# Optimization experiments

Hardware: AMD Instinct MI355X
Metric: run time of the kernel (lower is better)

## Reference

```python
import jax, jax.numpy as jnp
import numpy as np

NUM_HEADS = 6
ATTN_TH = 0.0
NEG_INF = -10000.0  # masked-score fill for threshold pruning


def setup_inputs() -> dict:
    key = jax.random.key(0)
    k1, k2, k3 = jax.random.split(key, 3)
    B, N, C = 8, 1024, 384
    x = jax.random.normal(k1, (B, N, C), dtype=jnp.float32)
    # Linear weights (torch layout: [out, in]), scaled like default init
    w_qkv = jax.random.normal(k2, (3 * C, C), dtype=jnp.float32) * (1.0 / np.sqrt(C))
    b_qkv = jnp.zeros((3 * C,), dtype=jnp.float32)
    w_proj = jax.random.normal(k3, (C, C), dtype=jnp.float32) * (1.0 / np.sqrt(C))
    b_proj = jnp.zeros((C,), dtype=jnp.float32)
    return {"x": x, "w_qkv": w_qkv, "b_qkv": b_qkv, "w_proj": w_proj, "b_proj": b_proj}


def reference(x, w_qkv, b_qkv, w_proj, b_proj):
    B, N, C = x.shape
    H = NUM_HEADS
    D = C // H
    scale = D ** -0.5
    # QAct nodes are identity (quant=False); QLinear is a plain linear.
    qkv = jnp.einsum('bnc,oc->bno', x, w_qkv) + b_qkv          # [B,N,3C]
    qkv = qkv.reshape(B, N, 3, H, D).transpose(2, 0, 3, 1, 4)   # [3,B,H,N,D]
    q, k, v = qkv[0], qkv[1], qkv[2]
    attn = jnp.einsum('bhnd,bhmd->bhnm', q, k) * scale          # [B,H,N,N]
    # Threshold pruning: scores below Attn_Th are masked out of the softmax.
    attn = jnp.where(attn < ATTN_TH, NEG_INF, attn)
    attn = jax.nn.softmax(attn, axis=-1)
    out = jnp.einsum('bhnm,bhmd->bhnd', attn, v)                # [B,H,N,D]
    out = out.transpose(0, 2, 1, 3).reshape(B, N, C)
    out = jnp.einsum('bnc,oc->bno', out, w_proj) + b_proj
    return out
```

## Files before the change

### kernel.cpp

```cpp
#include <hip/hip_runtime.h>
#include <hip/hip_bf16.h>


typedef __attribute__((__ext_vector_type__(8))) __bf16 bf16x8;
typedef __attribute__((__ext_vector_type__(8))) unsigned short ushort8;
typedef __attribute__((__ext_vector_type__(4))) unsigned short ushort4v;
typedef __attribute__((__ext_vector_type__(4))) short short4v;
typedef __attribute__((__ext_vector_type__(4))) float f32x4;

#define NX 3145728
#define NQ 442368
#define NP 147456

__device__ __forceinline__ f32x4 mfma32(bf16x8 a, bf16x8 b, f32x4 c) {
    return __builtin_amdgcn_mfma_f32_16x16x32_bf16(a, b, c, 0, 0, 0);
}
__device__ __forceinline__ f32x4 mfma16(short4v a, short4v b, f32x4 c) {
    return __builtin_amdgcn_mfma_f32_16x16x16bf16_1k(a, b, c, 0, 0, 0);
}

__device__ __forceinline__ unsigned short f2bf(float f) {
    union { float f; unsigned int i; } x; x.f = f;
    unsigned int u = x.i;
    return (unsigned short)((u + 0x7fffu + ((u >> 16) & 1u)) >> 16);
}

__device__ __forceinline__ void dma16(const unsigned short* g, unsigned short* l) {
    __builtin_amdgcn_global_load_lds(
        (const __attribute__((address_space(1))) unsigned int*)g,
        (__attribute__((address_space(3))) unsigned int*)l, 16, 0, 0);
}

__global__ __launch_bounds__(256) void cvt_bf16(
    const float* __restrict__ x, const float* __restrict__ wq, const float* __restrict__ wp,
    unsigned short* __restrict__ xb, unsigned short* __restrict__ wqb, unsigned short* __restrict__ wpb)
{
    int i = blockIdx.x * 256 + threadIdx.x;
    const float* src; unsigned short* dst; int off;
    if (i < NX / 4)              { src = x;  dst = xb;  off = i * 4; }
    else if (i < (NX + NQ) / 4)  { src = wq; dst = wqb; off = i * 4 - NX; }
    else                         { src = wp; dst = wpb; off = i * 4 - NX - NQ; }
    float4 v = *(const float4*)(src + off);
    ushort4v r;
    r[0] = f2bf(v.x); r[1] = f2bf(v.y); r[2] = f2bf(v.z); r[3] = f2bf(v.w);
    *(ushort4v*)(dst + off) = r;
}

template <int MODE, int TM>
__global__ __launch_bounds__(TM * 2) void gemm_bt(
    const unsigned short* __restrict__ A,
    const unsigned short* __restrict__ B,
    const float* __restrict__ bias,
    unsigned short* __restrict__ qg,
    unsigned short* __restrict__ kg,
    unsigned short* __restrict__ vg,
    float* __restrict__ out,
    int M, int N, int K)
{
    const int tid  = threadIdx.x;
    const int lane = tid & 63;
    const int wave = tid >> 6;
    const int l15  = lane & 15;
    const int quad = lane >> 4;
    const int m0 = blockIdx.x * TM;
    const int n0 = blockIdx.y * 128;
    const int wm = (wave >> 1) * 64;
    const int wn = (wave & 1) * 64;

    __shared__ __align__(16) unsigned short As[TM * 32];
    __shared__ __align__(16) unsigned short Bs[128 * 32];

    f32x4 acc[4][4];
    #pragma unroll
    for (int i = 0; i < 4; ++i)
        #pragma unroll
        for (int j = 0; j < 4; ++j)
            acc[i][j] = (f32x4){0.f, 0.f, 0.f, 0.f};

    for (int k0 = 0; k0 < K; k0 += 32) {
        #pragma unroll
        for (int t = 0; t < 2; ++t) {
            int i = tid + t * TM * 2;
            dma16(A + (size_t)(m0 + (i >> 2)) * K + k0 + (i & 3) * 8,
                  As + t * TM * 16 + wave * 512);
        }
        #pragma unroll
        for (int t = 0; t < 512 / (TM * 2); ++t) {
            int i = tid + t * TM * 2;
            dma16(B + (size_t)(n0 + (i >> 2)) * K + k0 + (i & 3) * 8,
                  Bs + t * TM * 16 + wave * 512);
        }
        __syncthreads();

        bf16x8 af[4], bff[4];
        #pragma unroll
        for (int mt = 0; mt < 4; ++mt)
            af[mt] = *(const bf16x8*)(As + (wm + mt * 16 + l15) * 32 + quad * 8);
        #pragma unroll
        for (int nt = 0; nt < 4; ++nt)
            bff[nt] = *(const bf16x8*)(Bs + (wn + nt * 16 + l15) * 32 + quad * 8);
        #pragma unroll
        for (int mt = 0; mt < 4; ++mt)
            #pragma unroll
            for (int nt = 0; nt < 4; ++nt)
                acc[mt][nt] = mfma32(af[mt], bff[nt], acc[mt][nt]);
        __syncthreads();
    }

    if constexpr (MODE == 0) {
        if (n0 < 384) {
            #pragma unroll
            for (int nt = 0; nt < 4; ++nt) {
                int n = n0 + wn + nt * 16 + l15;
                float bv = bias[n];
                #pragma unroll
                for (int mt = 0; mt < 4; ++mt) {
                    int mbase = m0 + wm + mt * 16 + quad * 4;
                    #pragma unroll
                    for (int r = 0; r < 4; ++r)
                        qg[(size_t)(mbase + r) * 384 + n] = f2bf((acc[mt][nt][r] + bv) * 0.125f);
                }
            }
        } else if (n0 < 768) {
            #pragma unroll
            for (int nt = 0; nt < 4; ++nt) {
                int n = n0 + wn + nt * 16 + l15;
                float bv = bias[n];
                int c2 = n - 384;
                int h = c2 >> 6, ck = c2 & 63;
                int half = ck >> 5, qd = (ck >> 3) & 3, j = ck & 7;
                #pragma unroll
                for (int mt = 0; mt < 4; ++mt) {
                    int mbase = m0 + wm + mt * 16 + quad * 4;
                    #pragma unroll
                    for (int r = 0; r < 4; ++r) {
                        int tok = mbase + r;
                        int b = tok >> 10, kv = tok & 1023;
                        int kt = kv >> 4, lk = kv & 15;
                        kg[(size_t)(b * 6 + h) * 65536 +
                           ((((size_t)kt * 2 + half) * 4 + qd) * 16 + lk) * 8 + j]
                            = f2bf(acc[mt][nt][r] + bv);
                    }
                }
            }
        } else {
            #pragma unroll
            for (int nt = 0; nt < 4; ++nt) {
                int n = n0 + wn + nt * 16 + l15;
                float bv = bias[n];
                int c2 = n - 768;
                int h = c2 >> 6, d = c2 & 63;
                int dt = d >> 4, lv = d & 15;
                #pragma unroll
                for (int mt = 0; mt < 4; ++mt) {
                    int mbase = m0 + wm + mt * 16 + quad * 4;
                    int b = mbase >> 10, kvb = mbase & 1023;
                    int cc = kvb >> 6, jt = (kvb >> 4) & 3, qd = (kvb >> 2) & 3;
                    ushort4v pk;
                    #pragma unroll
                    for (int r = 0; r < 4; ++r) pk[r] = f2bf(acc[mt][nt][r] + bv);
                    *(ushort4v*)(vg + (size_t)(b * 6 + h) * 65536 + (size_t)cc * 4096 +
                                 (((jt * 4 + dt) * 4 + qd) * 16 + lv) * 4) = pk;
                }
            }
        }
    } else {
        #pragma unroll
        for (int nt = 0; nt < 4; ++nt) {
            int n = n0 + wn + nt * 16 + l15;
            float bv = bias[n];
            #pragma unroll
            for (int mt = 0; mt < 4; ++mt) {
                int mbase = m0 + wm + mt * 16 + quad * 4;
                #pragma unroll
                for (int r = 0; r < 4; ++r)
                    out[(size_t)(mbase + r) * N + n] = acc[mt][nt][r] + bv;
            }
        }
    }
}

__global__ __launch_bounds__(256) void attn_fused(
    const unsigned short* __restrict__ qg,
    const unsigned short* __restrict__ kg,
    const unsigned short* __restrict__ vg,
    unsigned short* __restrict__ aout)
{
    const int tid  = threadIdx.x;
    const int wave = tid >> 6;
    const int lane = tid & 63;
    const int l15  = lane & 15;
    const int quad = lane >> 4;
    const int qt = blockIdx.x;
    const int h  = blockIdx.y;
    const int b  = blockIdx.z;

    const size_t rowbase = (size_t)b * 1024;
    const unsigned short* Kslab = kg + (size_t)(b * 6 + h) * 65536;
    const unsigned short* Vslab = vg + (size_t)(b * 6 + h) * 65536;
    const int q0 = qt * 64 + wave * 16;

    __shared__ __align__(16) unsigned short Kb[4096];
    __shared__ __align__(16) unsigned short Vb[4096];

    bf16x8 aq0, aq1;
    {
        const unsigned short* qrow = qg + (rowbase + q0 + l15) * 384 + h * 64 + quad * 8;
        aq0 = *(const bf16x8*)qrow;
        aq1 = *(const bf16x8*)(qrow + 32);
    }

    f32x4 accO[4];
    #pragma unroll
    for (int dt = 0; dt < 4; ++dt) accO[dt] = (f32x4){0.f, 0.f, 0.f, 0.f};
    float lsum = 0.f;

    for (int c = 0; c < 16; ++c) {
        #pragma unroll
        for (int t = 0; t < 2; ++t) {
            int i = tid + t * 256;
            dma16(Kslab + (size_t)c * 4096 + i * 8, Kb + t * 2048 + wave * 512);
            dma16(Vslab + (size_t)c * 4096 + i * 8, Vb + t * 2048 + wave * 512);
        }
        __syncthreads();

        #pragma unroll
        for (int kt = 0; kt < 4; ++kt) {
            bf16x8 ka = *(const bf16x8*)(Kb + (((kt * 2 + 0) * 4 + quad) * 16 + l15) * 8);
            bf16x8 kb = *(const bf16x8*)(Kb + (((kt * 2 + 1) * 4 + quad) * 16 + l15) * 8);
            f32x4 z = (f32x4){0.f, 0.f, 0.f, 0.f};
            z = mfma32(ka, aq0, z);
            z = mfma32(kb, aq1, z);

            short4v p;
            #pragma unroll
            for (int r = 0; r < 4; ++r) {
                float s = z[r];
                s = (s < 0.f) ? 0.f : __expf(s);
                lsum += s;
                p[r] = (short)f2bf(s);
            }
            #pragma unroll
            for (int dt = 0; dt < 4; ++dt) {
                short4v vv = *(const short4v*)(Vb + (((kt * 4 + dt) * 4 + quad) * 16 + l15) * 4);
                accO[dt] = mfma16(vv, p, accO[dt]);
            }
        }
        __syncthreads();
    }

    lsum += __shfl_xor(lsum, 16, 64);
    lsum += __shfl_xor(lsum, 32, 64);
    float inv = 1.0f / lsum;

    unsigned short* orow = aout + (rowbase + q0 + l15) * 384 + h * 64 + quad * 4;
    #pragma unroll
    for (int dt = 0; dt < 4; ++dt) {
        ushort4v pk;
        #pragma unroll
        for (int r = 0; r < 4; ++r) pk[r] = f2bf(accO[dt][r] * inv);
        *(ushort4v*)(orow + dt * 16) = pk;
    }
}

extern "C" void kernel_launch(void* const* d_in, const int* in_sizes, int n_in,
                              void* d_out, int out_size, void* d_ws, size_t ws_size,
                              hipStream_t stream) {
    const float* x      = (const float*)d_in[0];
    const float* w_qkv  = (const float*)d_in[1];
    const float* b_qkv  = (const float*)d_in[2];
    const float* w_proj = (const float*)d_in[3];
    const float* b_proj = (const float*)d_in[4];
    float* out = (float*)d_out;

    unsigned short* qg   = (unsigned short*)d_ws;
    unsigned short* kgp  = qg   + (size_t)NX;
    unsigned short* vgp  = kgp  + (size_t)NX;
    unsigned short* aout = vgp  + (size_t)NX;
    unsigned short* xb   = aout + (size_t)NX;
    unsigned short* wqb  = xb   + (size_t)NX;
    unsigned short* wpb  = wqb  + (size_t)NQ;

    cvt_bf16<<<3648, 256, 0, stream>>>(x, w_qkv, w_proj, xb, wqb, wpb);
    gemm_bt<0, 256><<<dim3(32, 9), 512, 0, stream>>>(
        xb, wqb, b_qkv, qg, kgp, vgp, nullptr, 8192, 1152, 384);
    attn_fused<<<dim3(16, 6, 8), 256, 0, stream>>>(qg, kgp, vgp, aout);
    gemm_bt<1, 128><<<dim3(64, 3), 256, 0, stream>>>(
        aout, wpb, b_proj, nullptr, nullptr, nullptr, out, 8192, 384, 384);
}
```

Baseline: 132.6 us.

## Double-buffer LDS staging in GEMM and attention, reorder attention grid

Both the GEMM and the attention kernel now keep two LDS buffers and issue the DMA for the next K-chunk right after the barrier, before computing on the current one. This drops one __syncthreads per iteration and lets global-to-LDS loads overlap with MFMA work. The attention grid is flattened so that consecutive blocks cover different (batch, head) slabs for the same query tile, which changes how K/V slabs are spread across CUs and the cache. LDS usage doubles, which may lower occupancy.

```diff
diff --git a/kernel.cpp b/kernel.cpp
--- a/kernel.cpp
+++ b/kernel.cpp
@@ -67,8 +67,8 @@
     const int wm = (wave >> 1) * 64;
     const int wn = (wave & 1) * 64;
 
-    __shared__ __align__(16) unsigned short As[TM * 32];
-    __shared__ __align__(16) unsigned short Bs[128 * 32];
+    __shared__ __align__(16) unsigned short As[2 * TM * 32];
+    __shared__ __align__(16) unsigned short Bs[2 * 128 * 32];
 
     f32x4 acc[4][4];
     #pragma unroll
@@ -77,34 +77,41 @@
         for (int j = 0; j < 4; ++j)
             acc[i][j] = (f32x4){0.f, 0.f, 0.f, 0.f};
 
-    for (int k0 = 0; k0 < K; k0 += 32) {
+    auto stage = [&](int k0, int buf) {
         #pragma unroll
         for (int t = 0; t < 2; ++t) {
             int i = tid + t * TM * 2;
             dma16(A + (size_t)(m0 + (i >> 2)) * K + k0 + (i & 3) * 8,
-                  As + t * TM * 16 + wave * 512);
+                  As + buf * TM * 32 + t * TM * 16 + wave * 512);
         }
         #pragma unroll
         for (int t = 0; t < 512 / (TM * 2); ++t) {
             int i = tid + t * TM * 2;
             dma16(B + (size_t)(n0 + (i >> 2)) * K + k0 + (i & 3) * 8,
-                  Bs + t * TM * 16 + wave * 512);
-        }
+                  Bs + buf * 4096 + t * TM * 16 + wave * 512);
+        }
+    };
+
+    const int nk = K >> 5;
+    stage(0, 0);
+    for (int ki = 0; ki < nk; ++ki) {
         __syncthreads();
+        if (ki + 1 < nk) stage((ki + 1) << 5, (ki + 1) & 1);
+        const unsigned short* as = As + (ki & 1) * TM * 32;
+        const unsigned short* bs = Bs + (ki & 1) * 4096;
 
         bf16x8 af[4], bff[4];
         #pragma unroll
         for (int mt = 0; mt < 4; ++mt)
-            af[mt] = *(const bf16x8*)(As + (wm + mt * 16 + l15) * 32 + quad * 8);
+            af[mt] = *(const bf16x8*)(as + (wm + mt * 16 + l15) * 32 + quad * 8);
         #pragma unroll
         for (int nt = 0; nt < 4; ++nt)
-            bff[nt] = *(const bf16x8*)(Bs + (wn + nt * 16 + l15) * 32 + quad * 8);
+            bff[nt] = *(const bf16x8*)(bs + (wn + nt * 16 + l15) * 32 + quad * 8);
         #pragma unroll
         for (int mt = 0; mt < 4; ++mt)
             #pragma unroll
             for (int nt = 0; nt < 4; ++nt)
                 acc[mt][nt] = mfma32(af[mt], bff[nt], acc[mt][nt]);
-        __syncthreads();
     }
 
     if constexpr (MODE == 0) {
@@ -191,17 +198,19 @@
     const int lane = tid & 63;
     const int l15  = lane & 15;
     const int quad = lane >> 4;
-    const int qt = blockIdx.x;
-    const int h  = blockIdx.y;
-    const int b  = blockIdx.z;
+    const int id = blockIdx.x;
+    const int s  = id % 48;
+    const int qt = id / 48;
+    const int b  = s / 6;
+    const int h  = s % 6;
 
     const size_t rowbase = (size_t)b * 1024;
-    const unsigned short* Kslab = kg + (size_t)(b * 6 + h) * 65536;
-    const unsigned short* Vslab = vg + (size_t)(b * 6 + h) * 65536;
+    const unsigned short* Kslab = kg + (size_t)s * 65536;
+    const unsigned short* Vslab = vg + (size_t)s * 65536;
     const int q0 = qt * 64 + wave * 16;
 
-    __shared__ __align__(16) unsigned short Kb[4096];
-    __shared__ __align__(16) unsigned short Vb[4096];
+    __shared__ __align__(16) unsigned short Kb[2 * 4096];
+    __shared__ __align__(16) unsigned short Vb[2 * 4096];
 
     bf16x8 aq0, aq1;
     {
@@ -215,38 +224,44 @@
     for (int dt = 0; dt < 4; ++dt) accO[dt] = (f32x4){0.f, 0.f, 0.f, 0.f};
     float lsum = 0.f;
 
-    for (int c = 0; c < 16; ++c) {
+    auto stage = [&](int c, int buf) {
         #pragma unroll
         for (int t = 0; t < 2; ++t) {
             int i = tid + t * 256;
-            dma16(Kslab + (size_t)c * 4096 + i * 8, Kb + t * 2048 + wave * 512);
-            dma16(Vslab + (size_t)c * 4096 + i * 8, Vb + t * 2048 + wave * 512);
-        }
+            dma16(Kslab + (size_t)c * 4096 + i * 8, Kb + buf * 4096 + t * 2048 + wave * 512);
+            dma16(Vslab + (size_t)c * 4096 + i * 8, Vb + buf * 4096 + t * 2048 + wave * 512);
+        }
+    };
+
+    stage(0, 0);
+    for (int c = 0; c < 16; ++c) {
         __syncthreads();
+        if (c + 1 < 16) stage(c + 1, (c + 1) & 1);
+        const unsigned short* kb = Kb + (c & 1) * 4096;
+        const unsigned short* vb = Vb + (c & 1) * 4096;
 
         #pragma unroll
         for (int kt = 0; kt < 4; ++kt) {
-            bf16x8 ka = *(const bf16x8*)(Kb + (((kt * 2 + 0) * 4 + quad) * 16 + l15) * 8);
-            bf16x8 kb = *(const bf16x8*)(Kb + (((kt * 2 + 1) * 4 + quad) * 16 + l15) * 8);
+            bf16x8 ka = *(const bf16x8*)(kb + (((kt * 2 + 0) * 4 + quad) * 16 + l15) * 8);
+            bf16x8 kbf = *(const bf16x8*)(kb + (((kt * 2 + 1) * 4 + quad) * 16 + l15) * 8);
             f32x4 z = (f32x4){0.f, 0.f, 0.f, 0.f};
             z = mfma32(ka, aq0, z);
-            z = mfma32(kb, aq1, z);
+            z = mfma32(kbf, aq1, z);
 
             short4v p;
             #pragma unroll
             for (int r = 0; r < 4; ++r) {
-                float s = z[r];
-                s = (s < 0.f) ? 0.f : __expf(s);
-                lsum += s;
-                p[r] = (short)f2bf(s);
+                float sc = z[r];
+                sc = (sc < 0.f) ? 0.f : __expf(sc);
+                lsum += sc;
+                p[r] = (short)f2bf(sc);
             }
             #pragma unroll
             for (int dt = 0; dt < 4; ++dt) {
-                short4v vv = *(const short4v*)(Vb + (((kt * 4 + dt) * 4 + quad) * 16 + l15) * 4);
+                short4v vv = *(const short4v*)(vb + (((kt * 4 + dt) * 4 + quad) * 16 + l15) * 4);
                 accO[dt] = mfma16(vv, p, accO[dt]);
             }
         }
-        __syncthreads();
     }
 
     lsum += __shfl_xor(lsum, 16, 64);
@@ -284,7 +299,7 @@
     cvt_bf16<<<3648, 256, 0, stream>>>(x, w_qkv, w_proj, xb, wqb, wpb);
     gemm_bt<0, 256><<<dim3(32, 9), 512, 0, stream>>>(
         xb, wqb, b_qkv, qg, kgp, vgp, nullptr, 8192, 1152, 384);
-    attn_fused<<<dim3(16, 6, 8), 256, 0, stream>>>(qg, kgp, vgp, aout);
+    attn_fused<<<768, 256, 0, stream>>>(qg, kgp, vgp, aout);
     gemm_bt<1, 128><<<dim3(64, 3), 256, 0, stream>>>(
         aout, wpb, b_proj, nullptr, nullptr, nullptr, out, 8192, 384, 384);
 }
```

Result: faster. 128.5 us (-3.1%).
